# Kernel optimization log

Hardware: AMD Instinct MI355X
Metric: run time of the kernel (lower is better)

## Reference

```python
import jax, jax.numpy as jnp
import numpy as np

D_MODEL = 1024
N_HEADS = 16
HEAD_DIM = D_MODEL // N_HEADS


def setup_inputs() -> dict:
    key = jax.random.key(0)
    ks = jax.random.split(key, 5)
    s = 0.02  # small init scale to keep softmax numerics reasonable
    x = jax.random.normal(ks[0], (4, 2048, D_MODEL), dtype=jnp.float32)
    w_qkv = jax.random.normal(ks[1], (D_MODEL, 3 * D_MODEL), dtype=jnp.float32) * s
    b_qkv = jnp.zeros((3 * D_MODEL,), dtype=jnp.float32)
    w_proj = jax.random.normal(ks[2], (D_MODEL, D_MODEL), dtype=jnp.float32) * s
    b_proj = jnp.zeros((D_MODEL,), dtype=jnp.float32)
    return {"x": x, "w_qkv": w_qkv, "b_qkv": b_qkv, "w_proj": w_proj, "b_proj": b_proj}


def reference(x, w_qkv, b_qkv, w_proj, b_proj):
    B, T, C = x.shape
    scale = 1.0 / np.sqrt(HEAD_DIM)
    qkv = x @ w_qkv + b_qkv                               # [B,T,3C]
    qkv = qkv.reshape(B, T, 3, N_HEADS, HEAD_DIM)
    q = qkv[:, :, 0].transpose(0, 2, 1, 3)               # [B,H,T,D]
    k = qkv[:, :, 1].transpose(0, 2, 1, 3)
    v = qkv[:, :, 2].transpose(0, 2, 1, 3)
    att = jnp.einsum('bhqd,bhkd->bhqk', q, k) * scale    # [B,H,T,T]
    causal = jnp.tril(jnp.ones((T, T), dtype=bool))
    att = jnp.where(causal, att, -jnp.inf)
    att = jax.nn.softmax(att, axis=-1)
    y = jnp.einsum('bhqk,bhkd->bhqd', att, v)            # [B,H,T,D]
    y = y.transpose(0, 2, 1, 3).reshape(B, T, C)
    y = y @ w_proj + b_proj
    return y
```

## Files before the change

kernel.cpp:

```cpp
#include <hip/hip_runtime.h>
#include <stdint.h>

#define BATCH 4
#define SEQ 2048
#define DMODEL 1024
#define NHEADS 16
#define HDIM 64
#define MROWS (BATCH * SEQ)

typedef float floatx4 __attribute__((ext_vector_type(4)));
typedef __bf16 bf16x8 __attribute__((ext_vector_type(8)));
typedef __bf16 bf16x4 __attribute__((ext_vector_type(4)));
typedef short short8 __attribute__((ext_vector_type(8)));

__device__ __forceinline__ unsigned short f32_to_bf16(float f) {
    union { float f; unsigned int u; } c; c.f = f;
    unsigned int u = c.u;
    unsigned int r = (u + 0x7FFFu + ((u >> 16) & 1u)) >> 16;
    return (unsigned short)r;
}

__device__ __forceinline__ void async_ld16(const void* g, void* l) {
    __builtin_amdgcn_global_load_lds(
        (const __attribute__((address_space(1))) unsigned int*)g,
        (__attribute__((address_space(3))) unsigned int*)l, 16, 0, 0);
}

__global__ __launch_bounds__(256) void conv_f32_bf16(
    const float* __restrict__ in, unsigned short* __restrict__ out, int n4) {
    int i = blockIdx.x * 256 + threadIdx.x;
    if (i < n4) {
        float4 v = ((const float4*)in)[i];
        ushort4 o;
        o.x = f32_to_bf16(v.x); o.y = f32_to_bf16(v.y);
        o.z = f32_to_bf16(v.z); o.w = f32_to_bf16(v.w);
        ((ushort4*)out)[i] = o;
    }
}

__global__ __launch_bounds__(256) void transp_conv(
    const float* __restrict__ in, unsigned short* __restrict__ out, int K, int N) {
    __shared__ float tile[32][33];
    int bx = blockIdx.x * 32;
    int by = blockIdx.y * 32;
    int tx = threadIdx.x, ty = threadIdx.y;
#pragma unroll
    for (int i = 0; i < 4; ++i)
        tile[ty + i * 8][tx] = in[(size_t)(by + ty + i * 8) * N + bx + tx];
    __syncthreads();
#pragma unroll
    for (int i = 0; i < 4; ++i)
        out[(size_t)(bx + ty + i * 8) * K + by + tx] = f32_to_bf16(tile[tx][ty + i * 8]);
}

__global__ __launch_bounds__(256) void transp_bf16_head(
    const unsigned short* __restrict__ in, unsigned short* __restrict__ out) {
    __shared__ unsigned short tile[32][33];
    const unsigned short* src = in + (size_t)blockIdx.z * SEQ * HDIM;
    unsigned short* dst = out + (size_t)blockIdx.z * SEQ * HDIM;
    int bx = blockIdx.x * 32;
    int by = blockIdx.y * 32;
    int tx = threadIdx.x, ty = threadIdx.y;
#pragma unroll
    for (int i = 0; i < 4; ++i)
        tile[ty + i * 8][tx] = src[(size_t)(by + ty + i * 8) * HDIM + bx + tx];
    __syncthreads();
#pragma unroll
    for (int i = 0; i < 4; ++i) {
        int keyg = by + tx;
        int col2 = (keyg & ~63) | (((keyg & 15) << 2) | ((keyg >> 4) & 3));
        dst[(size_t)(bx + ty + i * 8) * SEQ + col2] = tile[tx][ty + i * 8];
    }
}

template <int EPI>
__global__ __launch_bounds__(256) void gemm_bt(
    const unsigned short* __restrict__ A, const unsigned short* __restrict__ Bt,
    const float* __restrict__ bias, float* __restrict__ Cout,
    unsigned short* __restrict__ Qo, unsigned short* __restrict__ Ko,
    unsigned short* __restrict__ Vo, int M, int N, int K) {
    __shared__ __align__(16) unsigned short As[128 * 32];
    __shared__ __align__(16) unsigned short Bs[128 * 32];
    const int tid = threadIdx.x;
    const int lane = tid & 63;
    const int w = tid >> 6;
    const int wm = w & 1, wn = w >> 1;
    const int quad = lane >> 4, l16 = lane & 15;
    const int m0 = blockIdx.y * 128;
    const int n0 = blockIdx.x * 128;
    const int fsw = (l16 >> 1) & 3;

    floatx4 acc[4][4];
#pragma unroll
    for (int mt = 0; mt < 4; ++mt)
#pragma unroll
        for (int nt = 0; nt < 4; ++nt) acc[mt][nt] = (floatx4){0.f, 0.f, 0.f, 0.f};

    for (int k0 = 0; k0 < K; k0 += 32) {
#pragma unroll
        for (int r = 0; r < 2; ++r) {
            int idx = tid + r * 256;
            int row = idx >> 2;
            int cg = (idx & 3) ^ ((row >> 1) & 3);
            async_ld16(&A[(size_t)(m0 + row) * K + k0 + cg * 8], &As[idx * 8]);
            async_ld16(&Bt[(size_t)(n0 + row) * K + k0 + cg * 8], &Bs[idx * 8]);
        }
        __syncthreads();
        bf16x8 aF[4], bF[4];
#pragma unroll
        for (int mt = 0; mt < 4; ++mt)
            aF[mt] = *(const bf16x8*)&As[(wm * 64 + mt * 16 + l16) * 32 + (quad ^ fsw) * 8];
#pragma unroll
        for (int nt = 0; nt < 4; ++nt)
            bF[nt] = *(const bf16x8*)&Bs[(wn * 64 + nt * 16 + l16) * 32 + (quad ^ fsw) * 8];
#pragma unroll
        for (int mt = 0; mt < 4; ++mt)
#pragma unroll
            for (int nt = 0; nt < 4; ++nt)
                acc[mt][nt] = __builtin_amdgcn_mfma_f32_16x16x32_bf16(
                    aF[mt], bF[nt], acc[mt][nt], 0, 0, 0);
        __syncthreads();
    }

#pragma unroll
    for (int mt = 0; mt < 4; ++mt)
#pragma unroll
        for (int nt = 0; nt < 4; ++nt)
#pragma unroll
            for (int r = 0; r < 4; ++r) {
                int m = m0 + wm * 64 + mt * 16 + quad * 4 + r;
                int n = n0 + wn * 64 + nt * 16 + l16;
                float v = acc[mt][nt][r] + bias[n];
                if (EPI == 1) {
                    Cout[(size_t)m * N + n] = v;
                } else {
                    int sel = n >> 10, c = n & 1023;
                    int head = c >> 6, d = c & 63;
                    int bb = m >> 11, t = m & 2047;
                    unsigned short* dst = sel == 0 ? Qo : (sel == 1 ? Ko : Vo);
                    dst[((((size_t)bb * NHEADS + head) * SEQ + t) << 6) + d] = f32_to_bf16(v);
                }
            }
}

__global__ __launch_bounds__(256, 2) void attn_kernel(
    const unsigned short* __restrict__ Qg, const unsigned short* __restrict__ Kg,
    const unsigned short* __restrict__ Vtg, unsigned short* __restrict__ Yatt) {
    __shared__ __align__(16) unsigned short Kb2[2][4096];
    __shared__ __align__(16) unsigned short Vb2[2][4096];
    __shared__ __align__(16) unsigned short Ps[4][2048];

    const int tid = threadIdx.x;
    const int lane = tid & 63;
    const int w = tid >> 6;
    const int quad = lane >> 4, l16 = lane & 15;
    const int bh = blockIdx.x;
    const int by = blockIdx.y;
    const int sA = by * 4 + w;
    const size_t base = (size_t)bh * SEQ * HDIM;
    const int bIdx = bh >> 4, h = bh & 15;
    unsigned short* Pw = &Ps[w][0];
    const float csc = 0.18033688f;

    const int lrow = lane >> 3;
    const int lch = (lane & 7) ^ lrow;

    short8 osv = {0x3F80, 0x3F80, 0x3F80, 0x3F80, 0x3F80, 0x3F80, 0x3F80, 0x3F80};
    bf16x8 ones = __builtin_bit_cast(bf16x8, osv);

    for (int half = 0; half < 2; ++half) {
        const int rowb = (half == 0 ? sA : 63 - sA) * 32;
        const int kmaxB = (half == 0) ? (2 * by + 2) : (32 - 2 * by);

        bf16x8 qf[2][2];
#pragma unroll
        for (int mt = 0; mt < 2; ++mt)
#pragma unroll
            for (int kk = 0; kk < 2; ++kk)
                qf[mt][kk] = *(const bf16x8*)&Qg[base + (size_t)(rowb + mt * 16 + l16) * 64 +
                                                 kk * 32 + quad * 8];

        floatx4 lsum[2];
        floatx4 o[2][4];
#pragma unroll
        for (int mt = 0; mt < 2; ++mt) {
            lsum[mt] = (floatx4){0.f, 0.f, 0.f, 0.f};
#pragma unroll
            for (int nt = 0; nt < 4; ++nt) o[mt][nt] = (floatx4){0.f, 0.f, 0.f, 0.f};
        }

        {
            const unsigned short* Ktg = Kg + base;
            const unsigned short* Vtg_t = Vtg + base;
#pragma unroll
            for (int ii = 0; ii < 2; ++ii) {
                int i = w * 2 + ii;
                async_ld16(Ktg + (i * 8 + lrow) * 64 + lch * 8,
                           &Kb2[0][i * 512 + lane * 8]);
                async_ld16(Vtg_t + (size_t)(i * 8 + lrow) * SEQ + lch * 8,
                           &Vb2[0][i * 512 + lane * 8]);
            }
        }

        for (int kb = 0; kb < kmaxB; ++kb) {
            const int b = kb & 1;
            __syncthreads();

            if (kb + 1 < kmaxB) {
                const unsigned short* Ktg = Kg + base + (size_t)(kb + 1) * 64 * HDIM;
                const unsigned short* Vtg_t = Vtg + base + (kb + 1) * 64;
#pragma unroll
                for (int ii = 0; ii < 2; ++ii) {
                    int i = w * 2 + ii;
                    async_ld16(Ktg + (i * 8 + lrow) * 64 + lch * 8,
                               &Kb2[1 - b][i * 512 + lane * 8]);
                    async_ld16(Vtg_t + (size_t)(i * 8 + lrow) * SEQ + lch * 8,
                               &Vb2[1 - b][i * 512 + lane * 8]);
                }
            }

            floatx4 s[2][4];
#pragma unroll
            for (int mt = 0; mt < 2; ++mt)
#pragma unroll
                for (int nt = 0; nt < 4; ++nt) s[mt][nt] = (floatx4){0.f, 0.f, 0.f, 0.f};
#pragma unroll
            for (int kk = 0; kk < 2; ++kk) {
                bf16x8 kf[4];
#pragma unroll
                for (int nt = 0; nt < 4; ++nt)
                    kf[nt] = *(const bf16x8*)&Kb2[b][(nt * 16 + l16) * 64 +
                                                     ((kk * 4 + quad) ^ (l16 & 7)) * 8];
#pragma unroll
                for (int nt = 0; nt < 4; ++nt)
#pragma unroll
                    for (int mt = 0; mt < 2; ++mt)
                        s[mt][nt] = __builtin_amdgcn_mfma_f32_16x16x32_bf16(
                            qf[mt][kk], kf[nt], s[mt][nt], 0, 0, 0);
            }

            if ((kb * 64 + 63) > rowb) {
#pragma unroll
                for (int mt = 0; mt < 2; ++mt)
#pragma unroll
                    for (int nt = 0; nt < 4; ++nt)
#pragma unroll
                        for (int r = 0; r < 4; ++r) {
                            int key = kb * 64 + nt * 16 + l16;
                            int qrow = rowb + mt * 16 + quad * 4 + r;
                            if (key > qrow) s[mt][nt][r] = -INFINITY;
                        }
            }

#pragma unroll
            for (int mt = 0; mt < 2; ++mt)
#pragma unroll
                for (int nt = 0; nt < 4; ++nt)
#pragma unroll
                    for (int r = 0; r < 4; ++r)
                        s[mt][nt][r] = __builtin_amdgcn_exp2f(s[mt][nt][r] * csc);

#pragma unroll
            for (int mt = 0; mt < 2; ++mt)
#pragma unroll
                for (int r = 0; r < 4; ++r) {
                    int prow = mt * 16 + quad * 4 + r;
                    int unit = l16 ^ (prow & 14);
                    floatx4 t = {s[mt][0][r], s[mt][1][r], s[mt][2][r], s[mt][3][r]};
                    bf16x4 pv = __builtin_convertvector(t, bf16x4);
                    *(bf16x4*)&Pw[prow * 64 + unit * 4] = pv;
                }

#pragma unroll
            for (int kk = 0; kk < 2; ++kk) {
                bf16x8 af[2];
#pragma unroll
                for (int mt = 0; mt < 2; ++mt) {
                    int prow = mt * 16 + l16;
                    int u2 = (kk * 8 + quad * 2) ^ (l16 & 14);
                    af[mt] = *(const bf16x8*)&Pw[prow * 64 + u2 * 4];
                }
#pragma unroll
                for (int nt = 0; nt < 4; ++nt) {
                    bf16x8 vf = *(const bf16x8*)&Vb2[b][(nt * 16 + l16) * 64 +
                                                        ((kk * 4 + quad) ^ (l16 & 7)) * 8];
#pragma unroll
                    for (int mt = 0; mt < 2; ++mt)
                        o[mt][nt] = __builtin_amdgcn_mfma_f32_16x16x32_bf16(
                            af[mt], vf, o[mt][nt], 0, 0, 0);
                }
#pragma unroll
                for (int mt = 0; mt < 2; ++mt)
                    lsum[mt] = __builtin_amdgcn_mfma_f32_16x16x32_bf16(
                        af[mt], ones, lsum[mt], 0, 0, 0);
            }
        }

#pragma unroll
        for (int mt = 0; mt < 2; ++mt)
#pragma unroll
            for (int r = 0; r < 4; ++r) {
                float inv = 1.0f / lsum[mt][r];
                int qrow = rowb + mt * 16 + quad * 4 + r;
#pragma unroll
                for (int nt = 0; nt < 4; ++nt)
                    Yatt[((size_t)(bIdx * SEQ + qrow) << 10) + h * 64 + nt * 16 + l16] =
                        f32_to_bf16(o[mt][nt][r] * inv);
            }
    }
}

extern "C" void kernel_launch(void* const* d_in, const int* in_sizes, int n_in,
                              void* d_out, int out_size, void* d_ws, size_t ws_size,
                              hipStream_t stream) {
    const float* x = (const float*)d_in[0];
    const float* w_qkv = (const float*)d_in[1];
    const float* b_qkv = (const float*)d_in[2];
    const float* w_proj = (const float*)d_in[3];
    const float* b_proj = (const float*)d_in[4];
    float* out = (float*)d_out;

    char* ws = (char*)d_ws;
    unsigned short* xb     = (unsigned short*)(ws);
    unsigned short* wqkvT  = (unsigned short*)(ws + 16777216);
    unsigned short* wprojT = (unsigned short*)(ws + 23068672);
    unsigned short* Qb     = (unsigned short*)(ws + 25165824);
    unsigned short* Kb     = (unsigned short*)(ws + 41943040);
    unsigned short* Vb     = (unsigned short*)(ws + 58720256);
    unsigned short* Yatt   = (unsigned short*)(ws + 75497472);
    unsigned short* Vt     = (unsigned short*)(ws + 92274688);

    conv_f32_bf16<<<8192, 256, 0, stream>>>(x, xb, (MROWS * DMODEL) / 4);
    transp_conv<<<dim3(96, 32), dim3(32, 8), 0, stream>>>(w_qkv, wqkvT, DMODEL, 3 * DMODEL);
    transp_conv<<<dim3(32, 32), dim3(32, 8), 0, stream>>>(w_proj, wprojT, DMODEL, DMODEL);
    gemm_bt<0><<<dim3(24, 64), 256, 0, stream>>>(xb, wqkvT, b_qkv, nullptr, Qb, Kb, Vb,
                                                 MROWS, 3 * DMODEL, DMODEL);
    transp_bf16_head<<<dim3(2, 64, BATCH * NHEADS), dim3(32, 8), 0, stream>>>(Vb, Vt);
    attn_kernel<<<dim3(64, 8), 256, 0, stream>>>(Qb, Kb, Vt, Yatt);
    gemm_bt<1><<<dim3(8, 64), 256, 0, stream>>>(Yatt, wprojT, b_proj, out, nullptr, nullptr,
                                                nullptr, MROWS, DMODEL, DMODEL);
}
```

Baseline: 275.6 us.

## Double-buffer LDS tiles in bf16 GEMM to overlap async loads with MFMA

Converts the GEMM main loop to ping-pong shared-memory buffers. The next K-tile's async global-to-LDS loads are issued right after the barrier, so they run while the current tile's MFMAs execute. This also drops one barrier per iteration and hoists the per-thread address arithmetic out of the loop. The cost is twice the LDS footprint, which may lower occupancy.

```diff
diff --git a/kernel.cpp b/kernel.cpp
--- a/kernel.cpp
+++ b/kernel.cpp
@@ -79,8 +79,8 @@
     const float* __restrict__ bias, float* __restrict__ Cout,
     unsigned short* __restrict__ Qo, unsigned short* __restrict__ Ko,
     unsigned short* __restrict__ Vo, int M, int N, int K) {
-    __shared__ __align__(16) unsigned short As[128 * 32];
-    __shared__ __align__(16) unsigned short Bs[128 * 32];
+    __shared__ __align__(16) unsigned short As[2][128 * 32];
+    __shared__ __align__(16) unsigned short Bs[2][128 * 32];
     const int tid = threadIdx.x;
     const int lane = tid & 63;
     const int w = tid >> 6;
@@ -90,36 +90,52 @@
     const int n0 = blockIdx.x * 128;
     const int fsw = (l16 >> 1) & 3;
 
+    const int idx0 = tid, idx1 = tid + 256;
+    const int row0 = idx0 >> 2, row1 = idx1 >> 2;
+    const int cg0 = (idx0 & 3) ^ ((row0 >> 1) & 3);
+    const int cg1 = (idx1 & 3) ^ ((row1 >> 1) & 3);
+    const unsigned short* Ar0 = &A[(size_t)(m0 + row0) * K + cg0 * 8];
+    const unsigned short* Ar1 = &A[(size_t)(m0 + row1) * K + cg1 * 8];
+    const unsigned short* Br0 = &Bt[(size_t)(n0 + row0) * K + cg0 * 8];
+    const unsigned short* Br1 = &Bt[(size_t)(n0 + row1) * K + cg1 * 8];
+
     floatx4 acc[4][4];
 #pragma unroll
     for (int mt = 0; mt < 4; ++mt)
 #pragma unroll
         for (int nt = 0; nt < 4; ++nt) acc[mt][nt] = (floatx4){0.f, 0.f, 0.f, 0.f};
 
-    for (int k0 = 0; k0 < K; k0 += 32) {
-#pragma unroll
-        for (int r = 0; r < 2; ++r) {
-            int idx = tid + r * 256;
-            int row = idx >> 2;
-            int cg = (idx & 3) ^ ((row >> 1) & 3);
-            async_ld16(&A[(size_t)(m0 + row) * K + k0 + cg * 8], &As[idx * 8]);
-            async_ld16(&Bt[(size_t)(n0 + row) * K + k0 + cg * 8], &Bs[idx * 8]);
+    async_ld16(Ar0, &As[0][idx0 * 8]);
+    async_ld16(Br0, &Bs[0][idx0 * 8]);
+    async_ld16(Ar1, &As[0][idx1 * 8]);
+    async_ld16(Br1, &Bs[0][idx1 * 8]);
+
+    const int nk = K >> 5;
+    for (int kt = 0; kt < nk; ++kt) {
+        const int b = kt & 1;
+        __syncthreads();
+
+        if (kt + 1 < nk) {
+            const int ko = (kt + 1) << 5;
+            async_ld16(Ar0 + ko, &As[1 - b][idx0 * 8]);
+            async_ld16(Br0 + ko, &Bs[1 - b][idx0 * 8]);
+            async_ld16(Ar1 + ko, &As[1 - b][idx1 * 8]);
+            async_ld16(Br1 + ko, &Bs[1 - b][idx1 * 8]);
         }
-        __syncthreads();
+
         bf16x8 aF[4], bF[4];
 #pragma unroll
         for (int mt = 0; mt < 4; ++mt)
-            aF[mt] = *(const bf16x8*)&As[(wm * 64 + mt * 16 + l16) * 32 + (quad ^ fsw) * 8];
+            aF[mt] = *(const bf16x8*)&As[b][(wm * 64 + mt * 16 + l16) * 32 + (quad ^ fsw) * 8];
 #pragma unroll
         for (int nt = 0; nt < 4; ++nt)
-            bF[nt] = *(const bf16x8*)&Bs[(wn * 64 + nt * 16 + l16) * 32 + (quad ^ fsw) * 8];
+            bF[nt] = *(const bf16x8*)&Bs[b][(wn * 64 + nt * 16 + l16) * 32 + (quad ^ fsw) * 8];
 #pragma unroll
         for (int mt = 0; mt < 4; ++mt)
 #pragma unroll
             for (int nt = 0; nt < 4; ++nt)
                 acc[mt][nt] = __builtin_amdgcn_mfma_f32_16x16x32_bf16(
                     aF[mt], bF[nt], acc[mt][nt], 0, 0, 0);
-        __syncthreads();
     }
 
 #pragma unroll
```

Measured after the change: 266.9 us. -3.2%, faster.

## Replace GEMM with 256x256 double-buffered, software-pipelined 8-wave kernel

Applied to the files above, without the earlier changes.

Swaps the 128x128 single-buffered bf16 GEMM used for the QKV and output projections for a 256x256 tile kernel with 512 threads and a 64-wide K step. Global-to-LDS async loads are double-buffered and interleaved with MFMA phases, using explicit vmcnt waits, barriers and s_setprio. The aim is to raise data reuse per tile and hide memory latency behind MFMA work. In exchange it uses many more registers and much more LDS, which limits the kernel to one block per CU. The projection GEMM gets only 128 blocks, which may under-fill the 256 CUs.

```diff
diff --git a/kernel.cpp b/kernel.cpp
--- a/kernel.cpp
+++ b/kernel.cpp
@@ -25,6 +25,9 @@
         (const __attribute__((address_space(1))) unsigned int*)g,
         (__attribute__((address_space(3))) unsigned int*)l, 16, 0, 0);
 }
+
+#define BARRIER() do { asm volatile("" ::: "memory"); \
+    __builtin_amdgcn_s_barrier(); asm volatile("" ::: "memory"); } while (0)
 
 __global__ __launch_bounds__(256) void conv_f32_bf16(
     const float* __restrict__ in, unsigned short* __restrict__ out, int n4) {
@@ -74,71 +77,165 @@
 }
 
 template <int EPI>
-__global__ __launch_bounds__(256) void gemm_bt(
+__global__ __launch_bounds__(512, 1) void gemm256(
     const unsigned short* __restrict__ A, const unsigned short* __restrict__ Bt,
     const float* __restrict__ bias, float* __restrict__ Cout,
     unsigned short* __restrict__ Qo, unsigned short* __restrict__ Ko,
     unsigned short* __restrict__ Vo, int M, int N, int K) {
-    __shared__ __align__(16) unsigned short As[128 * 32];
-    __shared__ __align__(16) unsigned short Bs[128 * 32];
+    __shared__ __align__(16) unsigned short ldsA[2][2][8192];
+    __shared__ __align__(16) unsigned short ldsB[2][2][8192];
+
     const int tid = threadIdx.x;
     const int lane = tid & 63;
     const int w = tid >> 6;
-    const int wm = w & 1, wn = w >> 1;
+    const int wm = w >> 2, wn = w & 3;
     const int quad = lane >> 4, l16 = lane & 15;
-    const int m0 = blockIdx.y * 128;
-    const int n0 = blockIdx.x * 128;
-    const int fsw = (l16 >> 1) & 3;
-
-    floatx4 acc[4][4];
-#pragma unroll
-    for (int mt = 0; mt < 4; ++mt)
-#pragma unroll
-        for (int nt = 0; nt < 4; ++nt) acc[mt][nt] = (floatx4){0.f, 0.f, 0.f, 0.f};
-
-    for (int k0 = 0; k0 < K; k0 += 32) {
-#pragma unroll
-        for (int r = 0; r < 2; ++r) {
-            int idx = tid + r * 256;
-            int row = idx >> 2;
-            int cg = (idx & 3) ^ ((row >> 1) & 3);
-            async_ld16(&A[(size_t)(m0 + row) * K + k0 + cg * 8], &As[idx * 8]);
-            async_ld16(&Bt[(size_t)(n0 + row) * K + k0 + cg * 8], &Bs[idx * 8]);
-        }
-        __syncthreads();
-        bf16x8 aF[4], bF[4];
-#pragma unroll
-        for (int mt = 0; mt < 4; ++mt)
-            aF[mt] = *(const bf16x8*)&As[(wm * 64 + mt * 16 + l16) * 32 + (quad ^ fsw) * 8];
-#pragma unroll
-        for (int nt = 0; nt < 4; ++nt)
-            bF[nt] = *(const bf16x8*)&Bs[(wn * 64 + nt * 16 + l16) * 32 + (quad ^ fsw) * 8];
-#pragma unroll
-        for (int mt = 0; mt < 4; ++mt)
-#pragma unroll
-            for (int nt = 0; nt < 4; ++nt)
-                acc[mt][nt] = __builtin_amdgcn_mfma_f32_16x16x32_bf16(
-                    aF[mt], bF[nt], acc[mt][nt], 0, 0, 0);
-        __syncthreads();
+    const int m0 = blockIdx.y * 256;
+    const int n0 = blockIdx.x * 256;
+    const int ldb = K * 2;
+    const int NT = K >> 6;
+
+    const int t16 = tid * 16;
+    const int soff = t16 ^ (((t16 >> 9) & 1) << 5);
+    const int srow = soff >> 7;
+    const int scol = soff & 127;
+    const char* pAs = (const char*)A + (size_t)(m0 + srow) * ldb + scol;
+    const char* pBs = (const char*)Bt + (size_t)(n0 + srow) * ldb + scol;
+    char* ldA0 = (char*)&ldsA[0][0][0] + t16;
+    char* ldB0 = (char*)&ldsB[0][0][0] + t16;
+
+    auto stA = [&](int kt, int uu) {
+        async_ld16(pAs + (size_t)uu * 64 * ldb + kt * 128,
+                   ldA0 + ((kt & 1) << 15) + (uu << 13));
+    };
+    auto stB = [&](int kt, int uu) {
+        async_ld16(pBs + (size_t)uu * 64 * ldb + kt * 128,
+                   ldB0 + ((kt & 1) << 15) + (uu << 13));
+    };
+
+    const int xle = ((l16 >> 2) & 1) << 4;
+
+    floatx4 acc[8][4];
+#pragma unroll
+    for (int mf = 0; mf < 8; ++mf)
+#pragma unroll
+        for (int nf = 0; nf < 4; ++nf) acc[mf][nf] = (floatx4){0.f, 0.f, 0.f, 0.f};
+
+    stA(0, 0); stA(0, 1); stA(0, 2); stA(0, 3);
+    stB(0, 0); stB(0, 1); stB(0, 2); stB(0, 3);
+    if (NT > 1) {
+        stA(1, 0); stA(1, 2);
+        stB(1, 0); stB(1, 2);
+        stA(1, 1); stA(1, 3);
     }
 
-#pragma unroll
-    for (int mt = 0; mt < 4; ++mt)
-#pragma unroll
-        for (int nt = 0; nt < 4; ++nt)
+#define MFMA16(dst, af, bf) dst = __builtin_amdgcn_mfma_f32_16x16x32_bf16(af, bf, dst, 0, 0, 0)
+
+    for (int t = 0; t < NT; ++t) {
+        const int b = t & 1;
+        if (t + 1 < NT) asm volatile("s_waitcnt vmcnt(6)" ::: "memory");
+        else            asm volatile("s_waitcnt vmcnt(0)" ::: "memory");
+        BARRIER();
+
+        const unsigned short* Ab = &ldsA[b][wm][0];
+        const unsigned short* Bb = &ldsB[b][wn >> 1][(wn & 1) * 4096];
+
+        bf16x8 aR[4][2], bR[4][2];
+
+#pragma unroll
+        for (int mf = 0; mf < 4; ++mf)
+#pragma unroll
+            for (int kk = 0; kk < 2; ++kk)
+                aR[mf][kk] = *(const bf16x8*)&Ab[(mf * 16 + l16) * 64 +
+                                                 ((kk * 32 + quad * 8) ^ xle)];
+#pragma unroll
+        for (int nf = 0; nf < 2; ++nf)
+#pragma unroll
+            for (int kk = 0; kk < 2; ++kk)
+                bR[nf][kk] = *(const bf16x8*)&Bb[(nf * 16 + l16) * 64 +
+                                                 ((kk * 32 + quad * 8) ^ xle)];
+        if (t + 1 < NT) { stB(t + 1, 1); stB(t + 1, 3); }
+        BARRIER();
+        __builtin_amdgcn_s_setprio(1);
+#pragma unroll
+        for (int mf = 0; mf < 4; ++mf)
+#pragma unroll
+            for (int nf = 0; nf < 2; ++nf)
+#pragma unroll
+                for (int kk = 0; kk < 2; ++kk)
+                    MFMA16(acc[mf][nf], aR[mf][kk], bR[nf][kk]);
+        __builtin_amdgcn_s_setprio(0);
+        BARRIER();
+
+#pragma unroll
+        for (int nf = 2; nf < 4; ++nf)
+#pragma unroll
+            for (int kk = 0; kk < 2; ++kk)
+                bR[nf][kk] = *(const bf16x8*)&Bb[(nf * 16 + l16) * 64 +
+                                                 ((kk * 32 + quad * 8) ^ xle)];
+        if (t + 2 < NT) { stA(t + 2, 0); stA(t + 2, 2); }
+        BARRIER();
+        __builtin_amdgcn_s_setprio(1);
+#pragma unroll
+        for (int mf = 0; mf < 4; ++mf)
+#pragma unroll
+            for (int nf = 2; nf < 4; ++nf)
+#pragma unroll
+                for (int kk = 0; kk < 2; ++kk)
+                    MFMA16(acc[mf][nf], aR[mf][kk], bR[nf][kk]);
+        __builtin_amdgcn_s_setprio(0);
+        BARRIER();
+
+#pragma unroll
+        for (int mf = 0; mf < 4; ++mf)
+#pragma unroll
+            for (int kk = 0; kk < 2; ++kk)
+                aR[mf][kk] = *(const bf16x8*)&Ab[((mf + 4) * 16 + l16) * 64 +
+                                                 ((kk * 32 + quad * 8) ^ xle)];
+        if (t + 2 < NT) { stB(t + 2, 0); stB(t + 2, 2); }
+        BARRIER();
+        __builtin_amdgcn_s_setprio(1);
+#pragma unroll
+        for (int mf = 0; mf < 4; ++mf)
+#pragma unroll
+            for (int nf = 2; nf < 4; ++nf)
+#pragma unroll
+                for (int kk = 0; kk < 2; ++kk)
+                    MFMA16(acc[mf + 4][nf], aR[mf][kk], bR[nf][kk]);
+        __builtin_amdgcn_s_setprio(0);
+        BARRIER();
+
+        if (t + 2 < NT) { stA(t + 2, 1); stA(t + 2, 3); }
+        BARRIER();
+        __builtin_amdgcn_s_setprio(1);
+#pragma unroll
+        for (int mf = 0; mf < 4; ++mf)
+#pragma unroll
+            for (int nf = 0; nf < 2; ++nf)
+#pragma unroll
+                for (int kk = 0; kk < 2; ++kk)
+                    MFMA16(acc[mf + 4][nf], aR[mf][kk], bR[nf][kk]);
+        __builtin_amdgcn_s_setprio(0);
+    }
+#undef MFMA16
+
+#pragma unroll
+    for (int mf = 0; mf < 8; ++mf)
+#pragma unroll
+        for (int nf = 0; nf < 4; ++nf)
 #pragma unroll
             for (int r = 0; r < 4; ++r) {
-                int m = m0 + wm * 64 + mt * 16 + quad * 4 + r;
-                int n = n0 + wn * 64 + nt * 16 + l16;
-                float v = acc[mt][nt][r] + bias[n];
+                int m = m0 + wm * 128 + mf * 16 + quad * 4 + r;
+                int n = n0 + wn * 64 + nf * 16 + l16;
+                float v = acc[mf][nf][r] + bias[n];
                 if (EPI == 1) {
                     Cout[(size_t)m * N + n] = v;
                 } else {
                     int sel = n >> 10, c = n & 1023;
                     int head = c >> 6, d = c & 63;
-                    int bb = m >> 11, t = m & 2047;
+                    int bb = m >> 11, tt = m & 2047;
                     unsigned short* dst = sel == 0 ? Qo : (sel == 1 ? Ko : Vo);
-                    dst[((((size_t)bb * NHEADS + head) * SEQ + t) << 6) + d] = f32_to_bf16(v);
+                    dst[((((size_t)bb * NHEADS + head) * SEQ + tt) << 6) + d] = f32_to_bf16(v);
                 }
             }
 }
@@ -333,10 +430,10 @@
     conv_f32_bf16<<<8192, 256, 0, stream>>>(x, xb, (MROWS * DMODEL) / 4);
     transp_conv<<<dim3(96, 32), dim3(32, 8), 0, stream>>>(w_qkv, wqkvT, DMODEL, 3 * DMODEL);
     transp_conv<<<dim3(32, 32), dim3(32, 8), 0, stream>>>(w_proj, wprojT, DMODEL, DMODEL);
-    gemm_bt<0><<<dim3(24, 64), 256, 0, stream>>>(xb, wqkvT, b_qkv, nullptr, Qb, Kb, Vb,
+    gemm256<0><<<dim3(12, 32), 512, 0, stream>>>(xb, wqkvT, b_qkv, nullptr, Qb, Kb, Vb,
                                                  MROWS, 3 * DMODEL, DMODEL);
     transp_bf16_head<<<dim3(2, 64, BATCH * NHEADS), dim3(32, 8), 0, stream>>>(Vb, Vt);
     attn_kernel<<<dim3(64, 8), 256, 0, stream>>>(Qb, Kb, Vt, Yatt);
-    gemm_bt<1><<<dim3(8, 64), 256, 0, stream>>>(Yatt, wprojT, b_proj, out, nullptr, nullptr,
+    gemm256<1><<<dim3(4, 32), 512, 0, stream>>>(Yatt, wprojT, b_proj, out, nullptr, nullptr,
                                                 nullptr, MROWS, DMODEL, DMODEL);
 }
```

Result: no change. 276.3 us (+0.2%).
